# Kernel optimization log

Measured on AMD Instinct MI355X. Metric: run time of the kernel, lower is better.

## Reference

```python
import jax, jax.numpy as jnp
import numpy as np

B, D, DFF, E, TOPK = 16384, 512, 2048, 8, 2


def setup_inputs() -> dict:
    key = jax.random.key(0)
    ks = jax.random.split(key, 5)
    scale_g = 1.0 / np.sqrt(D)
    scale_1 = 1.0 / np.sqrt(D)
    scale_2 = 1.0 / np.sqrt(DFF)
    return {
        "x": jax.random.normal(ks[0], (B, D), dtype=jnp.float32),
        "Wg": jax.random.normal(ks[1], (D, E), dtype=jnp.float32) * scale_g,
        "W1": jax.random.normal(ks[2], (E, D, DFF), dtype=jnp.float32) * scale_1,
        "b1": jnp.zeros((E, DFF), dtype=jnp.float32),
        "W2": jax.random.normal(ks[3], (E, DFF, D), dtype=jnp.float32) * scale_2,
        "b2": jnp.zeros((E, D), dtype=jnp.float32),
    }


def reference(x, Wg, W1, b1, W2, b2):
    # --- gate: top-k softmax routing weights, zeros elsewhere ---
    logits = x @ Wg                              # [B, E]
    probs = jax.nn.softmax(logits, axis=-1)      # [B, E]
    vals, idx = jax.lax.top_k(probs, TOPK)       # [B, K], [B, K]
    routing = jnp.zeros_like(probs).at[jnp.arange(x.shape[0])[:, None], idx].set(vals)  # [B, E]

    # --- experts: dense FFN per expert (equivalent math to masked dispatch) ---
    # original: gather selected tokens per expert, compute, scatter into
    # zeros[E, B, D], multiply by routing.T[:, :, None], sum over experts.
    # routing weight is exactly 0 for unselected tokens, so the dense form
    # out = sum_e routing[b, e] * expert_e(x_b) computes identical results.
    h = jax.nn.relu(jnp.einsum('bd,edf->ebf', x, W1) + b1[:, None, :])  # [E, B, DFF]
    y = jnp.einsum('ebf,efd->ebd', h, W2) + b2[:, None, :]              # [E, B, D]
    out = jnp.einsum('ebd,be->bd', y, routing)                          # [B, D]
    return out
```

## Files before the change

kernel.cpp:

```cpp
#include <hip/hip_runtime.h>
#include <stdint.h>

#define BTOK 16384
#define DM   512
#define DFF  2048
#define NE   8
#define NPAIR (BTOK*2)
#define MAXT 288
#define TPXMAX 36

typedef short s16x8 __attribute__((ext_vector_type(8)));
typedef float f32x4 __attribute__((ext_vector_type(4)));

__device__ __forceinline__ uint16_t f2b(float f) {
  uint32_t u = __float_as_uint(f);
  u += 0x7fff + ((u >> 16) & 1);
  return (uint16_t)(u >> 16);
}

__device__ __forceinline__ void g2l16(const void* gp, void* lp) {
  __builtin_amdgcn_global_load_lds(
      (__attribute__((address_space(1))) void*)(void*)gp,
      (__attribute__((address_space(3))) void*)lp, 16, 0, 0);
}

__global__ void k_tr(const float* __restrict__ w1, const float* __restrict__ w2,
                     uint16_t* __restrict__ w1t, uint16_t* __restrict__ w2t) {
  __shared__ float t[32][33];
  int z = blockIdx.z, bx = blockIdx.x;
  int R, C, c0, r0;
  const float* src;
  uint16_t* dst;
  if (z < 8) { R = DM; C = DFF; c0 = (bx & 63) * 32; r0 = (bx >> 6) * 32;
               src = w1 + (size_t)z * R * C; dst = w1t + (size_t)z * R * C; }
  else       { R = DFF; C = DM; c0 = (bx & 15) * 32; r0 = (bx >> 4) * 32;
               src = w2 + (size_t)(z - 8) * R * C; dst = w2t + (size_t)(z - 8) * R * C; }
  int tx = threadIdx.x, ty = threadIdx.y;
#pragma unroll
  for (int j = 0; j < 4; j++)
    t[ty + j * 8][tx] = src[(size_t)(r0 + ty + j * 8) * C + c0 + tx];
  __syncthreads();
  int tid = ty * 32 + tx;
  int oc = tid >> 3, ch = tid & 7;
  if (ch < 4) {
    uint16_t v[8];
#pragma unroll
    for (int k = 0; k < 8; k++) v[k] = f2b(t[ch * 8 + k][oc]);
    *(s16x8*)(dst + (size_t)(c0 + oc) * R + r0 + ch * 8) = *(s16x8*)v;
  }
}

__global__ __launch_bounds__(256) void k_route(const float* __restrict__ x,
                                               const float* __restrict__ wg,
                                               int* __restrict__ counts,
                                               int* __restrict__ tk_e, float* __restrict__ tk_w,
                                               uint16_t* __restrict__ xb) {
  __shared__ int hist[NE];
  int tid = threadIdx.x, lane = tid & 63, wave = tid >> 6;
  if (tid < NE) hist[tid] = 0;
  __syncthreads();

  float wv[8][8];
#pragma unroll
  for (int j = 0; j < 8; j++) {
    const float4* wr = (const float4*)(wg + (size_t)(j * 64 + lane) * NE);
    float4 a = wr[0], b = wr[1];
    wv[j][0] = a.x; wv[j][1] = a.y; wv[j][2] = a.z; wv[j][3] = a.w;
    wv[j][4] = b.x; wv[j][5] = b.y; wv[j][6] = b.z; wv[j][7] = b.w;
  }

  int tok0 = blockIdx.x * 64 + wave * 16;
  for (int tt = 0; tt < 16; tt++) {
    int tok = tok0 + tt;
    const float* xr = x + (size_t)tok * DM;
    float xv[8];
#pragma unroll
    for (int j = 0; j < 8; j++) xv[j] = xr[j * 64 + lane];
    float acc[NE];
#pragma unroll
    for (int e = 0; e < NE; e++) acc[e] = 0.f;
#pragma unroll
    for (int j = 0; j < 8; j++)
#pragma unroll
      for (int e = 0; e < NE; e++) acc[e] += xv[j] * wv[j][e];
#pragma unroll
    for (int e = 0; e < NE; e++) {
#pragma unroll
      for (int off = 32; off > 0; off >>= 1) acc[e] += __shfl_xor(acc[e], off, 64);
    }
    if (lane == 0) {
      float mx = acc[0];
      for (int e = 1; e < NE; e++) mx = fmaxf(mx, acc[e]);
      float p[NE], s = 0.f;
      for (int e = 0; e < NE; e++) { p[e] = __expf(acc[e] - mx); s += p[e]; }
      float inv = 1.f / s;
      int e0 = 0; float v0 = p[0];
      for (int e = 1; e < NE; e++) if (p[e] > v0) { v0 = p[e]; e0 = e; }
      int e1 = -1; float v1 = -1.f;
      for (int e = 0; e < NE; e++) if (e != e0 && p[e] > v1) { v1 = p[e]; e1 = e; }
      tk_e[tok * 2]     = e0; tk_w[tok * 2]     = v0 * inv;
      tk_e[tok * 2 + 1] = e1; tk_w[tok * 2 + 1] = v1 * inv;
      atomicAdd(&hist[e0], 1);
      atomicAdd(&hist[e1], 1);
    }
  }
  const float* xs = x + (size_t)blockIdx.x * 32768;
  uint16_t* xd = xb + (size_t)blockIdx.x * 32768;
#pragma unroll
  for (int i = 0; i < 16; i++) {
    int o = i * 2048 + tid * 8;
    float4 a = *(const float4*)(xs + o);
    float4 b = *(const float4*)(xs + o + 4);
    uint16_t v[8] = {f2b(a.x), f2b(a.y), f2b(a.z), f2b(a.w),
                     f2b(b.x), f2b(b.y), f2b(b.z), f2b(b.w)};
    *(s16x8*)(xd + o) = *(s16x8*)v;
  }
  __syncthreads();
  if (tid < NE) atomicAdd(&counts[tid], hist[tid]);
}

__global__ void k_setup(const int* __restrict__ counts, int* __restrict__ offsets,
                        int* __restrict__ trB, int* __restrict__ texp, int* __restrict__ ntB) {
  __shared__ int soff[NE + 1], ts[NE + 1];
  int tid = threadIdx.x;
  if (tid == 0) {
    int off = 0;
    for (int e = 0; e < NE; e++) { soff[e] = off; offsets[e] = off; off += counts[e]; }
    soff[NE] = off; offsets[NE] = off;
    int nt = 0;
    for (int e = 0; e < NE; e++) { ts[e] = nt; nt += (counts[e] + 127) >> 7; }
    ts[NE] = nt; *ntB = nt;
  }
  __syncthreads();
  if (tid < NE) {
    int e = tid, base = ts[e], o = soff[e];
    int n = ts[e + 1] - ts[e];
    for (int i = 0; i < n; i++) { trB[base + i] = o + i * 128; texp[base + i] = e; }
  }
}

__global__ __launch_bounds__(256) void k_build(const int* __restrict__ tk_e, const float* __restrict__ tk_w,
                                               const int* __restrict__ offsets, int* __restrict__ cursors,
                                               int* __restrict__ tok_of, float* __restrict__ w_of) {
  __shared__ int lcnt[NE], lbase[NE];
  int tid = threadIdx.x;
  int i = blockIdx.x * 256 + tid;
  if (tid < NE) lcnt[tid] = 0;
  __syncthreads();
  int e = tk_e[i];
  int local = atomicAdd(&lcnt[e], 1);
  __syncthreads();
  if (tid < NE) lbase[tid] = atomicAdd(&cursors[tid], lcnt[tid]);
  __syncthreads();
  int slot = offsets[e] + lbase[e] + local;
  tok_of[slot] = i >> 1;
  w_of[slot] = tk_w[i];
}


#define LDS16(off) (*(const s16x8*)((const char*)smem + (off)))
#define VM6 asm volatile("s_waitcnt vmcnt(6)" ::: "memory")
#define VM0 asm volatile("s_waitcnt vmcnt(0)" ::: "memory")
#define NOVM do{}while(0)
#define NOSTG do{}while(0)
#define MFMA16 __builtin_amdgcn_mfma_f32_16x16x32_bf16
#define BSTR 24576

#define DS0_P(bb) do{ \
  bf0 = LDS16(offB0 + (bb)*BSTR); bf1 = LDS16(offB1 + (bb)*BSTR); \
  bf2 = LDS16(offB2 + (bb)*BSTR); bf3 = LDS16(offB3 + (bb)*BSTR); \
  bf4 = LDS16(offB4 + (bb)*BSTR); bf5 = LDS16(offB5 + (bb)*BSTR); \
  bf6 = LDS16(offB6 + (bb)*BSTR); bf7 = LDS16(offB7 + (bb)*BSTR); \
  af0 = LDS16(offA0 + (bb)*BSTR); af1 = LDS16(offA1 + (bb)*BSTR); }while(0)
#define DS1_P(bb) do{ \
  af2 = LDS16(offA2 + (bb)*BSTR); af3 = LDS16(offA3 + (bb)*BSTR); }while(0)
#define SA_P(bb) do{ \
  g2l16(gA0, (char*)smem + (bb)*BSTR + wave*1024); \
  g2l16(gA1, (char*)smem + (bb)*BSTR + 4096 + wave*1024); \
  gA0 += 32; gA1 += 32; }while(0)
#define SB_P(bb) do{ \
  g2l16(gB0, (char*)smem + (bb)*BSTR + 8192 + wave*1024); \
  g2l16(gB1, (char*)smem + (bb)*BSTR + 12288 + wave*1024); \
  g2l16(gB2, (char*)smem + (bb)*BSTR + 16384 + wave*1024); \
  g2l16(gB3, (char*)smem + (bb)*BSTR + 20480 + wave*1024); \
  gB0 += 32; gB1 += 32; gB2 += 32; gB3 += 32; }while(0)
#define MM16A do{ \
  __builtin_amdgcn_s_setprio(1); \
  acc[0][0] = MFMA16(af0, bf0, acc[0][0], 0, 0, 0); \
  acc[1][0] = MFMA16(af1, bf0, acc[1][0], 0, 0, 0); \
  acc[0][1] = MFMA16(af0, bf1, acc[0][1], 0, 0, 0); \
  acc[1][1] = MFMA16(af1, bf1, acc[1][1], 0, 0, 0); \
  acc[0][2] = MFMA16(af0, bf2, acc[0][2], 0, 0, 0); \
  acc[1][2] = MFMA16(af1, bf2, acc[1][2], 0, 0, 0); \
  acc[0][3] = MFMA16(af0, bf3, acc[0][3], 0, 0, 0); \
  acc[1][3] = MFMA16(af1, bf3, acc[1][3], 0, 0, 0); \
  acc[0][4] = MFMA16(af0, bf4, acc[0][4], 0, 0, 0); \
  acc[1][4] = MFMA16(af1, bf4, acc[1][4], 0, 0, 0); \
  acc[0][5] = MFMA16(af0, bf5, acc[0][5], 0, 0, 0); \
  acc[1][5] = MFMA16(af1, bf5, acc[1][5], 0, 0, 0); \
  acc[0][6] = MFMA16(af0, bf6, acc[0][6], 0, 0, 0); \
  acc[1][6] = MFMA16(af1, bf6, acc[1][6], 0, 0, 0); \
  acc[0][7] = MFMA16(af0, bf7, acc[0][7], 0, 0, 0); \
  acc[1][7] = MFMA16(af1, bf7, acc[1][7], 0, 0, 0); \
  __builtin_amdgcn_s_setprio(0); }while(0)
#define MM16B do{ \
  __builtin_amdgcn_s_setprio(1); \
  acc[2][0] = MFMA16(af2, bf0, acc[2][0], 0, 0, 0); \
  acc[3][0] = MFMA16(af3, bf0, acc[3][0], 0, 0, 0); \
  acc[2][1] = MFMA16(af2, bf1, acc[2][1], 0, 0, 0); \
  acc[3][1] = MFMA16(af3, bf1, acc[3][1], 0, 0, 0); \
  acc[2][2] = MFMA16(af2, bf2, acc[2][2], 0, 0, 0); \
  acc[3][2] = MFMA16(af3, bf2, acc[3][2], 0, 0, 0); \
  acc[2][3] = MFMA16(af2, bf3, acc[2][3], 0, 0, 0); \
  acc[3][3] = MFMA16(af3, bf3, acc[3][3], 0, 0, 0); \
  acc[2][4] = MFMA16(af2, bf4, acc[2][4], 0, 0, 0); \
  acc[3][4] = MFMA16(af3, bf4, acc[3][4], 0, 0, 0); \
  acc[2][5] = MFMA16(af2, bf5, acc[2][5], 0, 0, 0); \
  acc[3][5] = MFMA16(af3, bf5, acc[3][5], 0, 0, 0); \
  acc[2][6] = MFMA16(af2, bf6, acc[2][6], 0, 0, 0); \
  acc[3][6] = MFMA16(af3, bf6, acc[3][6], 0, 0, 0); \
  acc[2][7] = MFMA16(af2, bf7, acc[2][7], 0, 0, 0); \
  acc[3][7] = MFMA16(af3, bf7, acc[3][7], 0, 0, 0); \
  __builtin_amdgcn_s_setprio(0); }while(0)
#define TILEP(bb, SA, SB, VMX) do{ \
  DS0_P(bb); SA; \
  __builtin_amdgcn_s_barrier(); \
  asm volatile("s_waitcnt lgkmcnt(0)" ::: "memory"); \
  MM16A; \
  __builtin_amdgcn_s_barrier(); \
  DS1_P(bb); SB; \
  __builtin_amdgcn_s_barrier(); \
  asm volatile("s_waitcnt lgkmcnt(0)" ::: "memory"); \
  MM16B; \
  VMX; \
  __builtin_amdgcn_s_barrier(); }while(0)

#define GEOM_SETUP \
  int tid = threadIdx.x, lane = tid & 63, wave = tid >> 6; \
  int wm = wave >> 1, wn = wave & 1; \
  int l15 = lane & 15, l4 = lane >> 4; \
  int offA0, offA1, offA2, offA3; \
  int offB0, offB1, offB2, offB3, offB4, offB5, offB6, offB7; \
  { int r; \
    r = wm*64 + 0*16 + l15; offA0 = r*64 + ((l4 ^ ((r>>1)&3)) << 4); \
    r = wm*64 + 1*16 + l15; offA1 = r*64 + ((l4 ^ ((r>>1)&3)) << 4); \
    r = wm*64 + 2*16 + l15; offA2 = r*64 + ((l4 ^ ((r>>1)&3)) << 4); \
    r = wm*64 + 3*16 + l15; offA3 = r*64 + ((l4 ^ ((r>>1)&3)) << 4); \
    r = wn*128 + 0*16 + l15; offB0 = 8192 + r*64 + ((l4 ^ ((r>>1)&3)) << 4); \
    r = wn*128 + 1*16 + l15; offB1 = 8192 + r*64 + ((l4 ^ ((r>>1)&3)) << 4); \
    r = wn*128 + 2*16 + l15; offB2 = 8192 + r*64 + ((l4 ^ ((r>>1)&3)) << 4); \
    r = wn*128 + 3*16 + l15; offB3 = 8192 + r*64 + ((l4 ^ ((r>>1)&3)) << 4); \
    r = wn*128 + 4*16 + l15; offB4 = 8192 + r*64 + ((l4 ^ ((r>>1)&3)) << 4); \
    r = wn*128 + 5*16 + l15; offB5 = 8192 + r*64 + ((l4 ^ ((r>>1)&3)) << 4); \
    r = wn*128 + 6*16 + l15; offB6 = 8192 + r*64 + ((l4 ^ ((r>>1)&3)) << 4); \
    r = wn*128 + 7*16 + l15; offB7 = 8192 + r*64 + ((l4 ^ ((r>>1)&3)) << 4); \
  } \
  int rp = tid >> 2, cp = (tid & 3) ^ ((rp >> 1) & 3);

#define ACC_INIT \
  f32x4 acc[4][8]; \
  _Pragma("unroll") for (int m = 0; m < 4; m++) \
  _Pragma("unroll") for (int n = 0; n < 8; n++) \
  _Pragma("unroll") for (int i = 0; i < 4; i++) acc[m][n][i] = 0.f; \
  s16x8 af0, af1, af2, af3, bf0, bf1, bf2, bf3, bf4, bf5, bf6, bf7;

__global__ __launch_bounds__(256, 2) void k_gemm1(
    const uint16_t* __restrict__ xb, const uint16_t* __restrict__ w1t,
    const float* __restrict__ b1,
    const int* __restrict__ tok_of, const int* __restrict__ offsets,
    const int* __restrict__ trB, const int* __restrict__ texp, const int* __restrict__ ntB,
    uint16_t* __restrict__ h) {
  __shared__ __align__(16) uint16_t smem[36864];
  int id = blockIdx.x;
  int nt = *ntB, tpx = (nt + 7) >> 3;
  int x = id & 7, q = id >> 3, j = q >> 3;
  if (j >= tpx) return;
  int tile = x * tpx + j;
  if (tile >= nt) return;
  int n0 = (q & 7) * 256;
  int e = texp[tile], row0 = trB[tile], end = offsets[e + 1];
  GEOM_SETUP;

  const uint16_t *gA0, *gA1, *gB0, *gB1, *gB2, *gB3;
  { int s0 = row0 + rp;      if (s0 >= end) s0 = end - 1;
    int s1 = row0 + rp + 64; if (s1 >= end) s1 = end - 1;
    gA0 = xb + (size_t)tok_of[s0] * DM + cp * 8;
    gA1 = xb + (size_t)tok_of[s1] * DM + cp * 8; }
  { const uint16_t* wb = w1t + (size_t)e * DFF * DM;
    gB0 = wb + (size_t)(n0 + rp +   0) * DM + cp * 8;
    gB1 = wb + (size_t)(n0 + rp +  64) * DM + cp * 8;
    gB2 = wb + (size_t)(n0 + rp + 128) * DM + cp * 8;
    gB3 = wb + (size_t)(n0 + rp + 192) * DM + cp * 8; }

  ACC_INIT;

  SA_P(0); SB_P(0); SA_P(1); SB_P(1);
  VM6;
  __builtin_amdgcn_s_barrier();

#pragma unroll 1
  for (int g = 0; g < 4; ++g) {
    TILEP(0, SA_P(2), SB_P(2), VM6);
    TILEP(1, SA_P(0), SB_P(0), VM6);
    TILEP(2, SA_P(1), SB_P(1), VM6);
  }
  TILEP(0, SA_P(2), SB_P(2), VM6);
  TILEP(1, SA_P(0), SB_P(0), VM6);
  TILEP(2, NOSTG, NOSTG, VM0);
  TILEP(0, NOSTG, NOSTG, NOVM);

  {
    float bv[8];
#pragma unroll
    for (int n = 0; n < 8; n++) bv[n] = b1[(size_t)e * DFF + n0 + wn * 128 + n * 16 + l15];
    char* wrg = (char*)smem + wave * 4608;
    int rr = lane >> 2, cb = lane & 3;
#pragma unroll
    for (int m = 0; m < 4; m++) {
#pragma unroll
      for (int n = 0; n < 8; n++)
#pragma unroll
        for (int i = 0; i < 4; i++) {
          float v = fmaxf(acc[m][n][i] + bv[n], 0.f);
          *(uint16_t*)(wrg + (l4 * 4 + i) * 272 + (n * 16 + l15) * 2) = f2b(v);
        }
      int gr = row0 + wm * 64 + m * 16 + rr;
      const char* src = wrg + rr * 272 + cb * 64;
      if (gr < end) {
        uint16_t* dst = h + (size_t)gr * DFF + n0 + wn * 128 + cb * 32;
        *(s16x8*)(dst +  0) = *(const s16x8*)(src +  0);
        *(s16x8*)(dst +  8) = *(const s16x8*)(src + 16);
        *(s16x8*)(dst + 16) = *(const s16x8*)(src + 32);
        *(s16x8*)(dst + 24) = *(const s16x8*)(src + 48);
      }
    }
  }
}

__global__ __launch_bounds__(256, 2) void k_gemm2(
    const uint16_t* __restrict__ h, const uint16_t* __restrict__ w2t,
    const float* __restrict__ b2, const float* __restrict__ w_of,
    const int* __restrict__ tok_of, const int* __restrict__ offsets,
    const int* __restrict__ trB, const int* __restrict__ texp, const int* __restrict__ ntB,
    float* __restrict__ out) {
  __shared__ __align__(16) uint16_t smem[36864];
  int id = blockIdx.x;
  int nt = *ntB, tpx = (nt + 7) >> 3;
  int x = id & 7, q = id >> 3, j = q >> 1;
  if (j >= tpx) return;
  int tile = x * tpx + j;
  if (tile >= nt) return;
  int n0 = (q & 1) * 256;
  int e = texp[tile], row0 = trB[tile], end = offsets[e + 1];
  GEOM_SETUP;

  const uint16_t *gA0, *gA1, *gB0, *gB1, *gB2, *gB3;
  { int s0 = row0 + rp;      if (s0 >= end) s0 = end - 1;
    int s1 = row0 + rp + 64; if (s1 >= end) s1 = end - 1;
    gA0 = h + (size_t)s0 * DFF + cp * 8;
    gA1 = h + (size_t)s1 * DFF + cp * 8; }
  { const uint16_t* wb = w2t + (size_t)e * DM * DFF;
    gB0 = wb + (size_t)(n0 + rp +   0) * DFF + cp * 8;
    gB1 = wb + (size_t)(n0 + rp +  64) * DFF + cp * 8;
    gB2 = wb + (size_t)(n0 + rp + 128) * DFF + cp * 8;
    gB3 = wb + (size_t)(n0 + rp + 192) * DFF + cp * 8; }

  ACC_INIT;

  SA_P(0); SB_P(0); SA_P(1); SB_P(1);
  VM6;
  __builtin_amdgcn_s_barrier();

#pragma unroll 1
  for (int g = 0; g < 20; ++g) {
    TILEP(0, SA_P(2), SB_P(2), VM6);
    TILEP(1, SA_P(0), SB_P(0), VM6);
    TILEP(2, SA_P(1), SB_P(1), VM6);
  }
  TILEP(0, SA_P(2), SB_P(2), VM6);
  TILEP(1, SA_P(0), SB_P(0), VM6);
  TILEP(2, NOSTG, NOSTG, VM0);
  TILEP(0, NOSTG, NOSTG, NOVM);

  {
    float bv[8];
#pragma unroll
    for (int n = 0; n < 8; n++) bv[n] = b2[(size_t)e * DM + n0 + wn * 128 + n * 16 + l15];
#pragma unroll
    for (int m = 0; m < 4; m++)
#pragma unroll
      for (int i = 0; i < 4; i++) {
        int slot = row0 + wm * 64 + m * 16 + l4 * 4 + i;
        if (slot < end) {
          float wgt = w_of[slot];
          int tok = tok_of[slot];
          float* ob = out + (size_t)tok * DM + n0 + wn * 128 + l15;
#pragma unroll
          for (int n = 0; n < 8; n++) atomicAdd(ob + n * 16, wgt * (acc[m][n][i] + bv[n]));
        }
      }
  }
}

extern "C" void kernel_launch(void* const* d_in, const int* in_sizes, int n_in,
                              void* d_out, int out_size, void* d_ws, size_t ws_size,
                              hipStream_t stream) {
  const float* x  = (const float*)d_in[0];
  const float* wg = (const float*)d_in[1];
  const float* w1 = (const float*)d_in[2];
  const float* b1 = (const float*)d_in[3];
  const float* w2 = (const float*)d_in[4];
  const float* b2 = (const float*)d_in[5];
  float* out = (float*)d_out;

  char* ws = (char*)d_ws;
  const size_t MB = 1024 * 1024;
  uint16_t* xb   = (uint16_t*)ws;
  uint16_t* w1t  = (uint16_t*)(ws + 16 * MB);
  uint16_t* w2t  = (uint16_t*)(ws + 32 * MB);
  uint16_t* hbuf = (uint16_t*)(ws + 48 * MB);
  int* ctrl = (int*)(ws + 176 * MB);
  int*   counts  = ctrl;
  int*   cursors = ctrl + 8;
  int*   offsets = ctrl + 16;
  int*   ntB     = ctrl + 32;
  int*   trB     = ctrl + 64;
  int*   texp    = ctrl + 384;
  int*   tk_e    = ctrl + 1024;
  float* tk_w    = (float*)(ctrl + 1024 + 32768);
  int*   tok_of  = ctrl + 1024 + 2 * 32768;
  float* w_of    = (float*)(ctrl + 1024 + 3 * 32768);

  hipMemsetAsync(counts, 0, 16 * sizeof(int), stream);
  hipMemsetAsync(d_out, 0, out_size, stream);

  k_route<<<BTOK / 64, 256, 0, stream>>>(x, wg, counts, tk_e, tk_w, xb);
  k_tr<<<dim3(1024, 1, 16), dim3(32, 8), 0, stream>>>(w1, w2, w1t, w2t);
  k_setup<<<1, 64, 0, stream>>>(counts, offsets, trB, texp, ntB);
  k_build<<<NPAIR / 256, 256, 0, stream>>>(tk_e, tk_w, offsets, cursors, tok_of, w_of);
  k_gemm1<<<8 * TPXMAX * 8, 256, 0, stream>>>(xb, w1t, b1, tok_of, offsets,
                                              trB, texp, ntB, hbuf);
  k_gemm2<<<8 * TPXMAX * 2, 256, 0, stream>>>(hbuf, w2t, b2, w_of, tok_of, offsets,
                                              trB, texp, ntB, out);
}
```

Before: 403.2 us.

## Replace atomic scatter in second GEMM with slot-ordered stores plus combine kernel

The second expert GEMM now writes weighted per-slot results densely into an fp32 scratch buffer instead of atomically adding into the output per token. A new inverse map from token pair to slot is recorded during the build step, and a combine kernel sums each token's two slot rows into the output, which also removes the output memset. This trades scattered global float atomics for coalesced stores, at the cost of an extra 32 MB write plus read pass and one more kernel launch.

```diff
diff --git a/kernel.cpp b/kernel.cpp
--- a/kernel.cpp
+++ b/kernel.cpp
@@ -141,7 +141,8 @@
 
 __global__ __launch_bounds__(256) void k_build(const int* __restrict__ tk_e, const float* __restrict__ tk_w,
                                                const int* __restrict__ offsets, int* __restrict__ cursors,
-                                               int* __restrict__ tok_of, float* __restrict__ w_of) {
+                                               int* __restrict__ tok_of, float* __restrict__ w_of,
+                                               int* __restrict__ inv) {
   __shared__ int lcnt[NE], lbase[NE];
   int tid = threadIdx.x;
   int i = blockIdx.x * 256 + tid;
@@ -155,6 +156,7 @@
   int slot = offsets[e] + lbase[e] + local;
   tok_of[slot] = i >> 1;
   w_of[slot] = tk_w[i];
+  inv[i] = slot;
 }
 
 
@@ -340,9 +342,9 @@
 __global__ __launch_bounds__(256, 2) void k_gemm2(
     const uint16_t* __restrict__ h, const uint16_t* __restrict__ w2t,
     const float* __restrict__ b2, const float* __restrict__ w_of,
-    const int* __restrict__ tok_of, const int* __restrict__ offsets,
+    const int* __restrict__ offsets,
     const int* __restrict__ trB, const int* __restrict__ texp, const int* __restrict__ ntB,
-    float* __restrict__ out) {
+    float* __restrict__ y32) {
   __shared__ __align__(16) uint16_t smem[36864];
   int id = blockIdx.x;
   int nt = *ntB, tpx = (nt + 7) >> 3;
@@ -393,13 +395,24 @@
         int slot = row0 + wm * 64 + m * 16 + l4 * 4 + i;
         if (slot < end) {
           float wgt = w_of[slot];
-          int tok = tok_of[slot];
-          float* ob = out + (size_t)tok * DM + n0 + wn * 128 + l15;
-#pragma unroll
-          for (int n = 0; n < 8; n++) atomicAdd(ob + n * 16, wgt * (acc[m][n][i] + bv[n]));
+          size_t base = (size_t)slot * DM + n0 + wn * 128 + l15;
+#pragma unroll
+          for (int n = 0; n < 8; n++) y32[base + n * 16] = wgt * (acc[m][n][i] + bv[n]);
         }
       }
   }
+}
+
+__global__ __launch_bounds__(256) void k_combine(const float* __restrict__ y32,
+                                                 const int* __restrict__ inv,
+                                                 float* __restrict__ out) {
+  int tid = threadIdx.x;
+  int tok = blockIdx.x * 2 + (tid >> 7);
+  int c4 = (tid & 127) * 4;
+  int s0 = inv[tok * 2], s1 = inv[tok * 2 + 1];
+  const float4 a = *(const float4*)(y32 + (size_t)s0 * DM + c4);
+  const float4 b = *(const float4*)(y32 + (size_t)s1 * DM + c4);
+  *(float4*)(out + (size_t)tok * DM + c4) = make_float4(a.x + b.x, a.y + b.y, a.z + b.z, a.w + b.w);
 }
 
 extern "C" void kernel_launch(void* const* d_in, const int* in_sizes, int n_in,
@@ -430,16 +443,18 @@
   float* tk_w    = (float*)(ctrl + 1024 + 32768);
   int*   tok_of  = ctrl + 1024 + 2 * 32768;
   float* w_of    = (float*)(ctrl + 1024 + 3 * 32768);
+  int*   inv     = ctrl + 1024 + 4 * 32768;
+  float* y32     = (float*)(ws + 177 * MB);
 
   hipMemsetAsync(counts, 0, 16 * sizeof(int), stream);
-  hipMemsetAsync(d_out, 0, out_size, stream);
 
   k_route<<<BTOK / 64, 256, 0, stream>>>(x, wg, counts, tk_e, tk_w, xb);
   k_tr<<<dim3(1024, 1, 16), dim3(32, 8), 0, stream>>>(w1, w2, w1t, w2t);
   k_setup<<<1, 64, 0, stream>>>(counts, offsets, trB, texp, ntB);
-  k_build<<<NPAIR / 256, 256, 0, stream>>>(tk_e, tk_w, offsets, cursors, tok_of, w_of);
+  k_build<<<NPAIR / 256, 256, 0, stream>>>(tk_e, tk_w, offsets, cursors, tok_of, w_of, inv);
   k_gemm1<<<8 * TPXMAX * 8, 256, 0, stream>>>(xb, w1t, b1, tok_of, offsets,
                                               trB, texp, ntB, hbuf);
-  k_gemm2<<<8 * TPXMAX * 2, 256, 0, stream>>>(hbuf, w2t, b2, w_of, tok_of, offsets,
-                                              trB, texp, ntB, out);
-}
+  k_gemm2<<<8 * TPXMAX * 2, 256, 0, stream>>>(hbuf, w2t, b2, w_of, offsets,
+                                              trB, texp, ntB, y32);
+  k_combine<<<BTOK / 2, 256, 0, stream>>>(y32, inv, out);
+}
```

Measured after the change: 383.1 us. -5.0%, faster.
